# Kernel optimization log

Hardware: AMD Instinct MI355X
Metric: run time of the kernel (lower is better)

## Reference

```python
import jax, jax.numpy as jnp
import numpy as np

LN_EPS = 1e-5
MASK_FILL = -1e9


def setup_inputs() -> dict:
    key = jax.random.key(0)
    ks = jax.random.split(key, 8)
    B, S, D = 32, 1024, 1280
    Dout = 1280
    emb = jax.random.normal(ks[0], (B, S, D), dtype=jnp.float32)
    mask = jnp.ones((B, S), dtype=jnp.int32)
    w = 0.02
    return {
        "embeddings": emb,
        "attention_mask": mask,
        "Wq": jax.random.normal(ks[1], (D, D), jnp.float32) * w,
        "bq": jnp.zeros((D,), jnp.float32),
        "Wk": jax.random.normal(ks[2], (D, D), jnp.float32) * w,
        "bk": jnp.zeros((D,), jnp.float32),
        "Wv": jax.random.normal(ks[3], (D, D), jnp.float32) * w,
        "bv": jnp.zeros((D,), jnp.float32),
        "Wo": jax.random.normal(ks[4], (Dout, D), jnp.float32) * w,
        "bo": jnp.zeros((Dout,), jnp.float32),
        "gamma": jnp.ones((Dout,), jnp.float32),
        "beta": jnp.zeros((Dout,), jnp.float32),
    }


def reference(embeddings, attention_mask, Wq, bq, Wk, bk, Wv, bv, Wo, bo, gamma, beta):
    # Original torch module computes full [B,S,S] self-attention but only
    # consumes context[:, 0, :]. Mathematically identical (same output and
    # same gradients) to computing attention for query row 0 only.
    B, S, D = embeddings.shape
    scale = D ** -0.5
    q0 = embeddings[:, 0, :] @ Wq.T + bq                      # [B, D]
    k = jnp.einsum("bsd,ed->bse", embeddings, Wk) + bk        # [B, S, D]
    v = jnp.einsum("bsd,ed->bse", embeddings, Wv) + bv        # [B, S, D]
    scores = jnp.einsum("bd,bsd->bs", q0, k) * scale          # [B, S]
    scores = jnp.where(attention_mask == 0, MASK_FILL, scores)
    weights = jax.nn.softmax(scores, axis=-1)                 # [B, S]
    ctx = jnp.einsum("bs,bsd->bd", weights, v)                # [B, D]
    # output projection: Linear -> LayerNorm -> ReLU (dropout = identity in eval)
    h = ctx @ Wo.T + bo                                       # [B, Dout]
    mu = jnp.mean(h, axis=-1, keepdims=True)
    var = jnp.mean(jnp.square(h - mu), axis=-1, keepdims=True)
    h = (h - mu) * jax.lax.rsqrt(var + LN_EPS) * gamma + beta
    return jax.nn.relu(h)
```

## Files before the change

### kernel.cpp

```cpp
#include <hip/hip_runtime.h>
#include <hip/hip_bf16.h>

constexpr int cB = 32;
constexpr int cS = 1024;
constexpr int cD = 1280;
constexpr int KC = 16;
constexpr int NKC = cD / KC;
constexpr int NNC = cD / 256;

#define LN_EPS 1e-5f
#define MASK_FILL -1e9f
#define SCALE 0.02795084971874737f

__global__ __launch_bounds__(256) void k_dotT(const float* __restrict__ A,
                                              size_t lda,
                                              const float* __restrict__ W,
                                              const float* __restrict__ bias,
                                              float* __restrict__ out) {
    int w = threadIdx.x >> 6, lane = threadIdx.x & 63;
    int gw = blockIdx.x * 4 + w;
    int n = gw >> 1;
    int bh = (gw & 1) * 16;
    int d0 = lane * 4;

    float4 wr[5];
#pragma unroll
    for (int it = 0; it < 5; ++it)
        wr[it] = *reinterpret_cast<const float4*>(W + (size_t)n * cD + it * 256 + d0);
    float bn = bias[n];

#pragma unroll
    for (int bi = 0; bi < 16; ++bi) {
        int b = bh + bi;
        const float* a = A + (size_t)b * lda + d0;
        float4 av[5];
#pragma unroll
        for (int it = 0; it < 5; ++it)
            av[it] = *reinterpret_cast<const float4*>(a + it * 256);
        float dot = 0.f;
#pragma unroll
        for (int it = 0; it < 5; ++it)
            dot += av[it].x * wr[it].x + av[it].y * wr[it].y
                 + av[it].z * wr[it].z + av[it].w * wr[it].w;
#pragma unroll
        for (int off = 32; off; off >>= 1) dot += __shfl_xor(dot, off, 64);
        if (lane == 0) out[b * cD + n] = dot + bn;
    }
}

__global__ __launch_bounds__(256) void k_mm_p1(const float* __restrict__ A,
                                               const float* __restrict__ B,
                                               float* __restrict__ part) {
    int t = threadIdx.x;
    int nc = blockIdx.x % NNC, kc = blockIdx.x / NNC;
    int n0 = nc * 256, k0 = kc * KC;

    float w[KC];
#pragma unroll
    for (int kk = 0; kk < KC; ++kk)
        w[kk] = B[(size_t)(k0 + kk) * cD + n0 + t];

#pragma unroll
    for (int b = 0; b < cB; ++b) {
        const float* Ab = A + (size_t)b * cD + k0;
        float a0 = 0.f, a1 = 0.f, a2 = 0.f, a3 = 0.f;
#pragma unroll
        for (int kk = 0; kk < KC; kk += 4) {
            a0 += Ab[kk + 0] * w[kk + 0];
            a1 += Ab[kk + 1] * w[kk + 1];
            a2 += Ab[kk + 2] * w[kk + 2];
            a3 += Ab[kk + 3] * w[kk + 3];
        }
        part[(size_t)kc * (cB * cD) + b * cD + n0 + t] = (a0 + a1) + (a2 + a3);
    }
}

__global__ __launch_bounds__(256) void k_mm_red_qb(const float* __restrict__ part,
                                                   const float* __restrict__ q0,
                                                   const float* __restrict__ bk,
                                                   float* __restrict__ qk,
                                                   float* __restrict__ qb) {
    if (blockIdx.x < 160) {
        int i = blockIdx.x * 256 + threadIdx.x;
        float s = 0.f;
#pragma unroll
        for (int c = 0; c < NKC; ++c) s += part[(size_t)c * (cB * cD) + i];
        qk[i] = s;
    } else {
        int w = threadIdx.x >> 6, lane = threadIdx.x & 63;
        int d0 = lane * 4;
        float4 bkr[5];
#pragma unroll
        for (int it = 0; it < 5; ++it)
            bkr[it] = *reinterpret_cast<const float4*>(bk + it * 256 + d0);
#pragma unroll
        for (int r = 0; r < 8; ++r) {
            int b = w * 8 + r;
            float dot = 0.f;
#pragma unroll
            for (int it = 0; it < 5; ++it) {
                float4 qv = *reinterpret_cast<const float4*>(q0 + b * cD + it * 256 + d0);
                dot += qv.x * bkr[it].x + qv.y * bkr[it].y
                     + qv.z * bkr[it].z + qv.w * bkr[it].w;
            }
#pragma unroll
            for (int off = 32; off; off >>= 1) dot += __shfl_xor(dot, off, 64);
            if (lane == 0) qb[b] = dot;
        }
    }
}

__global__ __launch_bounds__(256) void k_attn(const float* __restrict__ emb,
                                              const float* __restrict__ qk,
                                              const float* __restrict__ qb,
                                              const int* __restrict__ mask,
                                              float* __restrict__ pm,
                                              float* __restrict__ pl,
                                              float* __restrict__ pacc) {
    __shared__ float s_all[4][cD];
    __shared__ float s_m[4], s_l[4];
    int blk = blockIdx.x;
    int b = blk >> 5, sc = blk & 31;
    int w = threadIdx.x >> 6, lane = threadIdx.x & 63;
    int d0 = lane * 4;

    float4 qkr[5];
#pragma unroll
    for (int it = 0; it < 5; ++it)
        qkr[it] = *reinterpret_cast<const float4*>(qk + b * cD + it * 256 + d0);
    float qbv = qb[b];

    float m = -INFINITY, l = 0.f;
    float4 acc[5];
#pragma unroll
    for (int it = 0; it < 5; ++it) acc[it] = make_float4(0.f, 0.f, 0.f, 0.f);

    int s0 = sc * 32 + w * 8;
    for (int r = 0; r < 8; ++r) {
        int s = s0 + r;
        const float* e = emb + (size_t)(b * cS + s) * cD + d0;
        float4 er[5];
#pragma unroll
        for (int it = 0; it < 5; ++it)
            er[it] = *reinterpret_cast<const float4*>(e + it * 256);
        float dot = 0.f;
#pragma unroll
        for (int it = 0; it < 5; ++it)
            dot += er[it].x * qkr[it].x + er[it].y * qkr[it].y
                 + er[it].z * qkr[it].z + er[it].w * qkr[it].w;
#pragma unroll
        for (int off = 32; off; off >>= 1) dot += __shfl_xor(dot, off, 64);
        float scv = (mask[b * cS + s] == 0) ? MASK_FILL : (dot + qbv) * SCALE;
        if (scv > m) {
            float f = __expf(m - scv);
            l *= f;
#pragma unroll
            for (int it = 0; it < 5; ++it) {
                acc[it].x *= f; acc[it].y *= f; acc[it].z *= f; acc[it].w *= f;
            }
            m = scv;
        }
        float p = __expf(scv - m);
        l += p;
#pragma unroll
        for (int it = 0; it < 5; ++it) {
            acc[it].x += p * er[it].x; acc[it].y += p * er[it].y;
            acc[it].z += p * er[it].z; acc[it].w += p * er[it].w;
        }
    }

    if (lane == 0) { s_m[w] = m; s_l[w] = l; }
    __syncthreads();
    float M = fmaxf(fmaxf(s_m[0], s_m[1]), fmaxf(s_m[2], s_m[3]));
    float f = __expf(m - M);
#pragma unroll
    for (int it = 0; it < 5; ++it)
        *reinterpret_cast<float4*>(&s_all[w][it * 256 + d0]) =
            make_float4(acc[it].x * f, acc[it].y * f, acc[it].z * f, acc[it].w * f);
    __syncthreads();

    if (threadIdx.x == 0) {
        float lt = s_l[0] * __expf(s_m[0] - M) + s_l[1] * __expf(s_m[1] - M)
                 + s_l[2] * __expf(s_m[2] - M) + s_l[3] * __expf(s_m[3] - M);
        pm[blk] = M; pl[blk] = lt;
    }
#pragma unroll
    for (int j = 0; j < 5; ++j) {
        int d = j * 256 + threadIdx.x;
        pacc[(size_t)blk * cD + d] =
            s_all[0][d] + s_all[1][d] + s_all[2][d] + s_all[3][d];
    }
}

__global__ __launch_bounds__(256) void k_attn_red(const float* __restrict__ pm,
                                                  const float* __restrict__ pl,
                                                  const float* __restrict__ pacc,
                                                  float* __restrict__ ectx) {
    int b = blockIdx.x / 5, j = blockIdx.x % 5;
    int d = j * 256 + threadIdx.x;
    float M = -INFINITY;
    for (int i = 0; i < 32; ++i) M = fmaxf(M, pm[b * 32 + i]);
    float L = 0.f, a = 0.f;
    for (int i = 0; i < 32; ++i) {
        float wf = __expf(pm[b * 32 + i] - M);
        L += pl[b * 32 + i] * wf;
        a += wf * pacc[(size_t)(b * 32 + i) * cD + d];
    }
    ectx[b * cD + d] = a / L;
}

__global__ __launch_bounds__(256) void k_ln(const float* __restrict__ h,
                                            const float* __restrict__ gamma,
                                            const float* __restrict__ beta,
                                            float* __restrict__ out) {
    int b = blockIdx.x;
    __shared__ float red[8];
    int wid = threadIdx.x >> 6, lane = threadIdx.x & 63;
    float v[5];
    float sum = 0.f;
#pragma unroll
    for (int j = 0; j < 5; ++j) {
        v[j] = h[b * cD + threadIdx.x + 256 * j];
        sum += v[j];
    }
#pragma unroll
    for (int off = 32; off; off >>= 1) sum += __shfl_xor(sum, off, 64);
    if (lane == 0) red[wid] = sum;
    __syncthreads();
    float mu = (red[0] + red[1] + red[2] + red[3]) * (1.f / cD);
    float vs = 0.f;
#pragma unroll
    for (int j = 0; j < 5; ++j) { float t = v[j] - mu; vs += t * t; }
#pragma unroll
    for (int off = 32; off; off >>= 1) vs += __shfl_xor(vs, off, 64);
    if (lane == 0) red[4 + wid] = vs;
    __syncthreads();
    float var = (red[4] + red[5] + red[6] + red[7]) * (1.f / cD);
    float inv = rsqrtf(var + LN_EPS);
#pragma unroll
    for (int j = 0; j < 5; ++j) {
        int idx = threadIdx.x + 256 * j;
        float o = (v[j] - mu) * inv * gamma[idx] + beta[idx];
        out[b * cD + idx] = fmaxf(o, 0.f);
    }
}

extern "C" void kernel_launch(void* const* d_in, const int* in_sizes, int n_in,
                              void* d_out, int out_size, void* d_ws, size_t ws_size,
                              hipStream_t stream) {
    const float* emb   = (const float*)d_in[0];
    const int*   mask  = (const int*)d_in[1];
    const float* Wq    = (const float*)d_in[2];
    const float* bq    = (const float*)d_in[3];
    const float* Wk    = (const float*)d_in[4];
    const float* bk    = (const float*)d_in[5];
    const float* Wv    = (const float*)d_in[6];
    const float* bv    = (const float*)d_in[7];
    const float* Wo    = (const float*)d_in[8];
    const float* bo    = (const float*)d_in[9];
    const float* gamma = (const float*)d_in[10];
    const float* beta  = (const float*)d_in[11];

    float* ws   = (float*)d_ws;
    float* part = ws;
    float* q0   = part + NKC * cB * cD;
    float* qk   = q0 + cB * cD;
    float* qb   = qk + cB * cD;
    float* pm   = qb + cB;
    float* pl   = pm + 1024;
    float* pacc = pl + 1024;
    float* ectx = pacc + (size_t)1024 * cD;
    float* ctx  = ectx + cB * cD;
    float* h    = ctx + cB * cD;

    k_dotT<<<640, 256, 0, stream>>>(emb, (size_t)cS * cD, Wq, bq, q0);
    k_mm_p1<<<NNC * NKC, 256, 0, stream>>>(q0, Wk, part);
    k_mm_red_qb<<<161, 256, 0, stream>>>(part, q0, bk, qk, qb);
    k_attn<<<cB * 32, 256, 0, stream>>>(emb, qk, qb, mask, pm, pl, pacc);
    k_attn_red<<<160, 256, 0, stream>>>(pm, pl, pacc, ectx);
    k_dotT<<<640, 256, 0, stream>>>(ectx, (size_t)cD, Wv, bv, ctx);
    k_dotT<<<640, 256, 0, stream>>>(ctx, (size_t)cD, Wo, bo, h);
    k_ln<<<cB, 256, 0, stream>>>(h, gamma, beta, (float*)d_out);
}
```

Measured before the change: 346.7 us.

## Fuse pre- and post-attention stages into persistent kernels with grid barriers

Merges the Q projection, K-side matmul and reduction into one persistent kernel, and the attention reduction, V/O projections and LayerNorm into another. Stages are separated by a software grid-wide barrier built from atomics. This removes several kernel launches and the gaps between them. The cost is barrier overhead and reliance on all 640 blocks being co-resident, and deadlock is possible if they are not.

```diff
diff --git a/kernel.cpp b/kernel.cpp
--- a/kernel.cpp
+++ b/kernel.cpp
@@ -1,5 +1,4 @@
 #include <hip/hip_runtime.h>
-#include <hip/hip_bf16.h>
 
 constexpr int cB = 32;
 constexpr int cS = 1024;
@@ -7,18 +6,36 @@
 constexpr int KC = 16;
 constexpr int NKC = cD / KC;
 constexpr int NNC = cD / 256;
+constexpr int GB = 640;
 
 #define LN_EPS 1e-5f
 #define MASK_FILL -1e9f
 #define SCALE 0.02795084971874737f
 
-__global__ __launch_bounds__(256) void k_dotT(const float* __restrict__ A,
-                                              size_t lda,
-                                              const float* __restrict__ W,
-                                              const float* __restrict__ bias,
-                                              float* __restrict__ out) {
-    int w = threadIdx.x >> 6, lane = threadIdx.x & 63;
-    int gw = blockIdx.x * 4 + w;
+__device__ __forceinline__ void gbar(int* cnt, int* sense, int nblk, int ph) {
+    __syncthreads();
+    if (threadIdx.x == 0) {
+        __threadfence();
+        if (atomicAdd(cnt, 1) == nblk - 1) {
+            atomicExch(cnt, 0);
+            __threadfence();
+            atomicExch(sense, ph);
+        } else {
+            while (atomicAdd(sense, 0) < ph)
+                __builtin_amdgcn_s_sleep(32);
+        }
+        __threadfence();
+    }
+    __syncthreads();
+}
+
+__device__ __forceinline__ void dotT_wave(const float* __restrict__ A, size_t lda,
+                                          const float* __restrict__ W,
+                                          const float* __restrict__ bias,
+                                          float* __restrict__ out,
+                                          int bid, int tid) {
+    int w = tid >> 6, lane = tid & 63;
+    int gw = bid * 4 + w;
     int n = gw >> 1;
     int bh = (gw & 1) * 16;
     int d0 = lane * 4;
@@ -48,46 +65,54 @@
     }
 }
 
-__global__ __launch_bounds__(256) void k_mm_p1(const float* __restrict__ A,
-                                               const float* __restrict__ B,
-                                               float* __restrict__ part) {
-    int t = threadIdx.x;
-    int nc = blockIdx.x % NNC, kc = blockIdx.x / NNC;
-    int n0 = nc * 256, k0 = kc * KC;
-
-    float w[KC];
-#pragma unroll
-    for (int kk = 0; kk < KC; ++kk)
-        w[kk] = B[(size_t)(k0 + kk) * cD + n0 + t];
-
-#pragma unroll
-    for (int b = 0; b < cB; ++b) {
-        const float* Ab = A + (size_t)b * cD + k0;
-        float a0 = 0.f, a1 = 0.f, a2 = 0.f, a3 = 0.f;
-#pragma unroll
-        for (int kk = 0; kk < KC; kk += 4) {
-            a0 += Ab[kk + 0] * w[kk + 0];
-            a1 += Ab[kk + 1] * w[kk + 1];
-            a2 += Ab[kk + 2] * w[kk + 2];
-            a3 += Ab[kk + 3] * w[kk + 3];
-        }
-        part[(size_t)kc * (cB * cD) + b * cD + n0 + t] = (a0 + a1) + (a2 + a3);
-    }
-}
-
-__global__ __launch_bounds__(256) void k_mm_red_qb(const float* __restrict__ part,
-                                                   const float* __restrict__ q0,
-                                                   const float* __restrict__ bk,
-                                                   float* __restrict__ qk,
-                                                   float* __restrict__ qb) {
-    if (blockIdx.x < 160) {
-        int i = blockIdx.x * 256 + threadIdx.x;
+__global__ __launch_bounds__(256, 3) void k_pre(const float* __restrict__ emb,
+                                                const float* __restrict__ Wq,
+                                                const float* __restrict__ bq,
+                                                const float* __restrict__ Wk,
+                                                const float* __restrict__ bk,
+                                                float* __restrict__ q0,
+                                                float* __restrict__ part,
+                                                float* __restrict__ qk,
+                                                float* __restrict__ qb,
+                                                int* gsync) {
+    int bid = blockIdx.x, tid = threadIdx.x;
+    int* cnt = gsync;
+    int* sense = gsync + 32;
+
+    dotT_wave(emb, (size_t)cS * cD, Wq, bq, q0, bid, tid);
+    gbar(cnt, sense, GB, 1);
+
+    if (bid < NNC * NKC) {
+        int nc = bid % NNC, kc = bid / NNC;
+        int n0 = nc * 256, k0 = kc * KC;
+        float w[KC];
+#pragma unroll
+        for (int kk = 0; kk < KC; ++kk)
+            w[kk] = Wk[(size_t)(k0 + kk) * cD + n0 + tid];
+#pragma unroll
+        for (int b = 0; b < cB; ++b) {
+            const float* Ab = q0 + (size_t)b * cD + k0;
+            float a0 = 0.f, a1 = 0.f, a2 = 0.f, a3 = 0.f;
+#pragma unroll
+            for (int kk = 0; kk < KC; kk += 4) {
+                a0 += Ab[kk + 0] * w[kk + 0];
+                a1 += Ab[kk + 1] * w[kk + 1];
+                a2 += Ab[kk + 2] * w[kk + 2];
+                a3 += Ab[kk + 3] * w[kk + 3];
+            }
+            part[(size_t)kc * (cB * cD) + b * cD + n0 + tid] = (a0 + a1) + (a2 + a3);
+        }
+    }
+    gbar(cnt, sense, GB, 2);
+
+    if (bid < 160) {
+        int i = bid * 256 + tid;
         float s = 0.f;
 #pragma unroll
         for (int c = 0; c < NKC; ++c) s += part[(size_t)c * (cB * cD) + i];
         qk[i] = s;
-    } else {
-        int w = threadIdx.x >> 6, lane = threadIdx.x & 63;
+    } else if (bid == 160) {
+        int w = tid >> 6, lane = tid & 63;
         int d0 = lane * 4;
         float4 bkr[5];
 #pragma unroll
@@ -192,56 +217,75 @@
     }
 }
 
-__global__ __launch_bounds__(256) void k_attn_red(const float* __restrict__ pm,
-                                                  const float* __restrict__ pl,
-                                                  const float* __restrict__ pacc,
-                                                  float* __restrict__ ectx) {
-    int b = blockIdx.x / 5, j = blockIdx.x % 5;
-    int d = j * 256 + threadIdx.x;
-    float M = -INFINITY;
-    for (int i = 0; i < 32; ++i) M = fmaxf(M, pm[b * 32 + i]);
-    float L = 0.f, a = 0.f;
-    for (int i = 0; i < 32; ++i) {
-        float wf = __expf(pm[b * 32 + i] - M);
-        L += pl[b * 32 + i] * wf;
-        a += wf * pacc[(size_t)(b * 32 + i) * cD + d];
-    }
-    ectx[b * cD + d] = a / L;
-}
-
-__global__ __launch_bounds__(256) void k_ln(const float* __restrict__ h,
-                                            const float* __restrict__ gamma,
-                                            const float* __restrict__ beta,
-                                            float* __restrict__ out) {
-    int b = blockIdx.x;
+__global__ __launch_bounds__(256, 3) void k_post(const float* __restrict__ pm,
+                                                 const float* __restrict__ pl,
+                                                 const float* __restrict__ pacc,
+                                                 float* __restrict__ ectx,
+                                                 const float* __restrict__ Wv,
+                                                 const float* __restrict__ bv,
+                                                 float* __restrict__ ctx,
+                                                 const float* __restrict__ Wo,
+                                                 const float* __restrict__ bo,
+                                                 float* __restrict__ h,
+                                                 const float* __restrict__ gamma,
+                                                 const float* __restrict__ beta,
+                                                 float* __restrict__ out,
+                                                 int* gsync) {
     __shared__ float red[8];
-    int wid = threadIdx.x >> 6, lane = threadIdx.x & 63;
-    float v[5];
-    float sum = 0.f;
-#pragma unroll
-    for (int j = 0; j < 5; ++j) {
-        v[j] = h[b * cD + threadIdx.x + 256 * j];
-        sum += v[j];
-    }
-#pragma unroll
-    for (int off = 32; off; off >>= 1) sum += __shfl_xor(sum, off, 64);
-    if (lane == 0) red[wid] = sum;
-    __syncthreads();
-    float mu = (red[0] + red[1] + red[2] + red[3]) * (1.f / cD);
-    float vs = 0.f;
-#pragma unroll
-    for (int j = 0; j < 5; ++j) { float t = v[j] - mu; vs += t * t; }
-#pragma unroll
-    for (int off = 32; off; off >>= 1) vs += __shfl_xor(vs, off, 64);
-    if (lane == 0) red[4 + wid] = vs;
-    __syncthreads();
-    float var = (red[4] + red[5] + red[6] + red[7]) * (1.f / cD);
-    float inv = rsqrtf(var + LN_EPS);
-#pragma unroll
-    for (int j = 0; j < 5; ++j) {
-        int idx = threadIdx.x + 256 * j;
-        float o = (v[j] - mu) * inv * gamma[idx] + beta[idx];
-        out[b * cD + idx] = fmaxf(o, 0.f);
+    int bid = blockIdx.x, tid = threadIdx.x;
+    int* cnt = gsync;
+    int* sense = gsync + 32;
+
+    if (bid < 160) {
+        int b = bid / 5, j = bid % 5;
+        int d = j * 256 + tid;
+        float M = -INFINITY;
+        for (int i = 0; i < 32; ++i) M = fmaxf(M, pm[b * 32 + i]);
+        float L = 0.f, a = 0.f;
+        for (int i = 0; i < 32; ++i) {
+            float wf = __expf(pm[b * 32 + i] - M);
+            L += pl[b * 32 + i] * wf;
+            a += wf * pacc[(size_t)(b * 32 + i) * cD + d];
+        }
+        ectx[b * cD + d] = a / L;
+    }
+    gbar(cnt, sense, GB, 3);
+
+    dotT_wave(ectx, (size_t)cD, Wv, bv, ctx, bid, tid);
+    gbar(cnt, sense, GB, 4);
+
+    dotT_wave(ctx, (size_t)cD, Wo, bo, h, bid, tid);
+    gbar(cnt, sense, GB, 5);
+
+    if (bid < cB) {
+        int wid = tid >> 6, lane = tid & 63;
+        float v[5];
+        float sum = 0.f;
+#pragma unroll
+        for (int j = 0; j < 5; ++j) {
+            v[j] = h[bid * cD + tid + 256 * j];
+            sum += v[j];
+        }
+#pragma unroll
+        for (int off = 32; off; off >>= 1) sum += __shfl_xor(sum, off, 64);
+        if (lane == 0) red[wid] = sum;
+        __syncthreads();
+        float mu = (red[0] + red[1] + red[2] + red[3]) * (1.f / cD);
+        float vs = 0.f;
+#pragma unroll
+        for (int j = 0; j < 5; ++j) { float t = v[j] - mu; vs += t * t; }
+#pragma unroll
+        for (int off = 32; off; off >>= 1) vs += __shfl_xor(vs, off, 64);
+        if (lane == 0) red[4 + wid] = vs;
+        __syncthreads();
+        float var = (red[4] + red[5] + red[6] + red[7]) * (1.f / cD);
+        float inv = rsqrtf(var + LN_EPS);
+#pragma unroll
+        for (int j = 0; j < 5; ++j) {
+            int idx = tid + 256 * j;
+            float o = (v[j] - mu) * inv * gamma[idx] + beta[idx];
+            out[bid * cD + idx] = fmaxf(o, 0.f);
+        }
     }
 }
 
@@ -272,13 +316,12 @@
     float* ectx = pacc + (size_t)1024 * cD;
     float* ctx  = ectx + cB * cD;
     float* h    = ctx + cB * cD;
-
-    k_dotT<<<640, 256, 0, stream>>>(emb, (size_t)cS * cD, Wq, bq, q0);
-    k_mm_p1<<<NNC * NKC, 256, 0, stream>>>(q0, Wk, part);
-    k_mm_red_qb<<<161, 256, 0, stream>>>(part, q0, bk, qk, qb);
+    int*   gsy  = (int*)(h + cB * cD);
+
+    hipMemsetAsync(gsy, 0, 64 * sizeof(int), stream);
+
+    k_pre<<<GB, 256, 0, stream>>>(emb, Wq, bq, Wk, bk, q0, part, qk, qb, gsy);
     k_attn<<<cB * 32, 256, 0, stream>>>(emb, qk, qb, mask, pm, pl, pacc);
-    k_attn_red<<<160, 256, 0, stream>>>(pm, pl, pacc, ectx);
-    k_dotT<<<640, 256, 0, stream>>>(ectx, (size_t)cD, Wv, bv, ctx);
-    k_dotT<<<640, 256, 0, stream>>>(ctx, (size_t)cD, Wo, bo, h);
-    k_ln<<<cB, 256, 0, stream>>>(h, gamma, beta, (float*)d_out);
-}
+    k_post<<<GB, 256, 0, stream>>>(pm, pl, pacc, ectx, Wv, bv, ctx, Wo, bo, h,
+                                   gamma, beta, (float*)d_out, gsy);
+}
```

Measured after the change: 485.1 us. 39.9% more time.

## Stage 8-row embedding tiles in LDS and split attention into smaller blocks

Applied to the files above, without the earlier changes.

The attention kernel now copies an 8-row tile of embeddings into shared memory and computes the row scores from LDS. It then does a plain per-block softmax and a weighted column sum, replacing the per-wavefront online softmax with its cross-wave merge. The grid grows from 1024 to 4096 blocks, which adds parallelism. In exchange the partial-accumulator buffer becomes four times larger, so the reduction kernel reads and writes more memory and loops over 128 partials per batch instead of 32.

```diff
diff --git a/kernel.cpp b/kernel.cpp
--- a/kernel.cpp
+++ b/kernel.cpp
@@ -1,5 +1,4 @@
 #include <hip/hip_runtime.h>
-#include <hip/hip_bf16.h>
 
 constexpr int cB = 32;
 constexpr int cS = 1024;
@@ -7,6 +6,9 @@
 constexpr int KC = 16;
 constexpr int NKC = cD / KC;
 constexpr int NNC = cD / 256;
+constexpr int RB = 8;
+constexpr int NSC = cS / RB;
+constexpr int NPART = cB * NSC;
 
 #define LN_EPS 1e-5f
 #define MASK_FILL -1e9f
@@ -117,12 +119,13 @@
                                               float* __restrict__ pm,
                                               float* __restrict__ pl,
                                               float* __restrict__ pacc) {
-    __shared__ float s_all[4][cD];
-    __shared__ float s_m[4], s_l[4];
+    __shared__ float tile[RB * cD];
+    __shared__ float s_sc[RB];
     int blk = blockIdx.x;
-    int b = blk >> 5, sc = blk & 31;
-    int w = threadIdx.x >> 6, lane = threadIdx.x & 63;
+    int b = blk >> 7, sc = blk & (NSC - 1);
+    int tid = threadIdx.x, w = tid >> 6, lane = tid & 63;
     int d0 = lane * 4;
+    int s0 = sc * RB;
 
     float4 qkr[5];
 #pragma unroll
@@ -130,66 +133,51 @@
         qkr[it] = *reinterpret_cast<const float4*>(qk + b * cD + it * 256 + d0);
     float qbv = qb[b];
 
-    float m = -INFINITY, l = 0.f;
-    float4 acc[5];
-#pragma unroll
-    for (int it = 0; it < 5; ++it) acc[it] = make_float4(0.f, 0.f, 0.f, 0.f);
-
-    int s0 = sc * 32 + w * 8;
-    for (int r = 0; r < 8; ++r) {
-        int s = s0 + r;
-        const float* e = emb + (size_t)(b * cS + s) * cD + d0;
-        float4 er[5];
-#pragma unroll
-        for (int it = 0; it < 5; ++it)
-            er[it] = *reinterpret_cast<const float4*>(e + it * 256);
+    const float4* src = reinterpret_cast<const float4*>(
+        emb + ((size_t)b * cS + s0) * cD);
+    float4* dst = reinterpret_cast<float4*>(tile);
+#pragma unroll
+    for (int i = 0; i < 10; ++i)
+        dst[i * 256 + tid] = src[i * 256 + tid];
+    __syncthreads();
+
+#pragma unroll
+    for (int rr = 0; rr < 2; ++rr) {
+        int r = w * 2 + rr;
+        const float* trow = tile + r * cD + d0;
         float dot = 0.f;
 #pragma unroll
-        for (int it = 0; it < 5; ++it)
-            dot += er[it].x * qkr[it].x + er[it].y * qkr[it].y
-                 + er[it].z * qkr[it].z + er[it].w * qkr[it].w;
+        for (int it = 0; it < 5; ++it) {
+            float4 ev = *reinterpret_cast<const float4*>(trow + it * 256);
+            dot += ev.x * qkr[it].x + ev.y * qkr[it].y
+                 + ev.z * qkr[it].z + ev.w * qkr[it].w;
+        }
 #pragma unroll
         for (int off = 32; off; off >>= 1) dot += __shfl_xor(dot, off, 64);
-        float scv = (mask[b * cS + s] == 0) ? MASK_FILL : (dot + qbv) * SCALE;
-        if (scv > m) {
-            float f = __expf(m - scv);
-            l *= f;
-#pragma unroll
-            for (int it = 0; it < 5; ++it) {
-                acc[it].x *= f; acc[it].y *= f; acc[it].z *= f; acc[it].w *= f;
-            }
-            m = scv;
-        }
-        float p = __expf(scv - m);
-        l += p;
-#pragma unroll
-        for (int it = 0; it < 5; ++it) {
-            acc[it].x += p * er[it].x; acc[it].y += p * er[it].y;
-            acc[it].z += p * er[it].z; acc[it].w += p * er[it].w;
-        }
-    }
-
-    if (lane == 0) { s_m[w] = m; s_l[w] = l; }
-    __syncthreads();
-    float M = fmaxf(fmaxf(s_m[0], s_m[1]), fmaxf(s_m[2], s_m[3]));
-    float f = __expf(m - M);
-#pragma unroll
-    for (int it = 0; it < 5; ++it)
-        *reinterpret_cast<float4*>(&s_all[w][it * 256 + d0]) =
-            make_float4(acc[it].x * f, acc[it].y * f, acc[it].z * f, acc[it].w * f);
-    __syncthreads();
-
-    if (threadIdx.x == 0) {
-        float lt = s_l[0] * __expf(s_m[0] - M) + s_l[1] * __expf(s_m[1] - M)
-                 + s_l[2] * __expf(s_m[2] - M) + s_l[3] * __expf(s_m[3] - M);
-        pm[blk] = M; pl[blk] = lt;
-    }
+        if (lane == 0) s_sc[r] = dot;
+    }
+    __syncthreads();
+
+    float scv[RB], m = -INFINITY;
+#pragma unroll
+    for (int r = 0; r < RB; ++r) {
+        scv[r] = (mask[b * cS + s0 + r] == 0) ? MASK_FILL
+                                              : (s_sc[r] + qbv) * SCALE;
+        m = fmaxf(m, scv[r]);
+    }
+    float p[RB], l = 0.f;
+#pragma unroll
+    for (int r = 0; r < RB; ++r) { p[r] = __expf(scv[r] - m); l += p[r]; }
+
 #pragma unroll
     for (int j = 0; j < 5; ++j) {
-        int d = j * 256 + threadIdx.x;
-        pacc[(size_t)blk * cD + d] =
-            s_all[0][d] + s_all[1][d] + s_all[2][d] + s_all[3][d];
-    }
+        int col = j * 256 + tid;
+        float a = 0.f;
+#pragma unroll
+        for (int r = 0; r < RB; ++r) a += p[r] * tile[r * cD + col];
+        pacc[(size_t)blk * cD + col] = a;
+    }
+    if (tid == 0) { pm[blk] = m; pl[blk] = l; }
 }
 
 __global__ __launch_bounds__(256) void k_attn_red(const float* __restrict__ pm,
@@ -199,12 +187,12 @@
     int b = blockIdx.x / 5, j = blockIdx.x % 5;
     int d = j * 256 + threadIdx.x;
     float M = -INFINITY;
-    for (int i = 0; i < 32; ++i) M = fmaxf(M, pm[b * 32 + i]);
+    for (int i = 0; i < NSC; ++i) M = fmaxf(M, pm[b * NSC + i]);
     float L = 0.f, a = 0.f;
-    for (int i = 0; i < 32; ++i) {
-        float wf = __expf(pm[b * 32 + i] - M);
-        L += pl[b * 32 + i] * wf;
-        a += wf * pacc[(size_t)(b * 32 + i) * cD + d];
+    for (int i = 0; i < NSC; ++i) {
+        float wf = __expf(pm[b * NSC + i] - M);
+        L += pl[b * NSC + i] * wf;
+        a += wf * pacc[(size_t)(b * NSC + i) * cD + d];
     }
     ectx[b * cD + d] = a / L;
 }
@@ -267,16 +255,16 @@
     float* qk   = q0 + cB * cD;
     float* qb   = qk + cB * cD;
     float* pm   = qb + cB;
-    float* pl   = pm + 1024;
-    float* pacc = pl + 1024;
-    float* ectx = pacc + (size_t)1024 * cD;
+    float* pl   = pm + NPART;
+    float* pacc = pl + NPART;
+    float* ectx = pacc + (size_t)NPART * cD;
     float* ctx  = ectx + cB * cD;
     float* h    = ctx + cB * cD;
 
     k_dotT<<<640, 256, 0, stream>>>(emb, (size_t)cS * cD, Wq, bq, q0);
     k_mm_p1<<<NNC * NKC, 256, 0, stream>>>(q0, Wk, part);
     k_mm_red_qb<<<161, 256, 0, stream>>>(part, q0, bk, qk, qb);
-    k_attn<<<cB * 32, 256, 0, stream>>>(emb, qk, qb, mask, pm, pl, pacc);
+    k_attn<<<NPART, 256, 0, stream>>>(emb, qk, qb, mask, pm, pl, pacc);
     k_attn_red<<<160, 256, 0, stream>>>(pm, pl, pacc, ectx);
     k_dotT<<<640, 256, 0, stream>>>(ectx, (size_t)cD, Wv, bv, ctx);
     k_dotT<<<640, 256, 0, stream>>>(ctx, (size_t)cD, Wo, bo, h);
```

New measurement: 362.7 us. 4.6% more time.
